# Performance work log

Measured on AMD Instinct MI355X. Metric: run time of the kernel, lower is better.

## Reference

```python
import jax, jax.numpy as jnp
import numpy as np
import math

N = 524288          # number of 3D query points
L = 4               # grid_level = num_sin_layers - 2
F = 8               # feat_dim per hash level
T = 1 << 19         # log2_hashmap_size = 19 (hardcoded in module)
H = 64              # SIREN hidden width (dims entries)
OUT_DIM = 128       # sin_dims[-1] * size_factor
BOUND = 1.0
BASE_RES = 16.0
PER_LEVEL_SCALE = 2.0
BASE_SIGMA = 5.0
EXP_SIGMA = 2.0
SIN_W0 = 30.0
SIN_W1 = 30.0

_PRIMES = jnp.array([1, 2654435761, 805459861], dtype=jnp.uint32)  # tcnn hash primes
_CORNERS = np.array([[(i >> 2) & 1, (i >> 1) & 1, i & 1] for i in range(8)])
_CORNERS_U = jnp.asarray(_CORNERS, dtype=jnp.uint32)
_CORNERS_F = jnp.asarray(_CORNERS, dtype=jnp.float32)


def hash_grid(pos01, table):
    """Multi-resolution hash-grid encoding. pos01: [N,3] in [0,1], table: [L,T,F] -> [L,N,F]."""
    res = jnp.floor(BASE_RES * PER_LEVEL_SCALE ** jnp.arange(L, dtype=jnp.float32))  # [L]

    def level(tab, r):
        p = pos01 * r                       # [N,3]
        p0 = jnp.floor(p)
        f = p - p0                          # trilinear fractions
        c = p0.astype(jnp.uint32)[:, None, :] + _CORNERS_U[None]   # [N,8,3] corner coords
        hp = c * _PRIMES
        h = (hp[..., 0] ^ hp[..., 1] ^ hp[..., 2]) & jnp.uint32(T - 1)  # [N,8] hash indices
        feats = tab[h]                      # [N,8,F]
        w = jnp.prod(jnp.where(_CORNERS_F[None] > 0, f[:, None, :], 1.0 - f[:, None, :]), axis=-1)  # [N,8]
        return jnp.einsum('nc,ncf->nf', w, feats)

    return jax.vmap(level)(table, res)


def setup_inputs() -> dict:
    key = jax.random.key(0)
    ks = jax.random.split(key, 10)
    in_pos = jax.random.uniform(ks[0], (N, 3), minval=-BOUND, maxval=BOUND)
    table = jax.random.uniform(ks[1], (L, T, F), minval=-1e-4, maxval=1e-4)
    # ffn[i] = randn(F, H) * base_sigma * exp_sigma**i
    scales = BASE_SIGMA * EXP_SIGMA ** jnp.arange(L, dtype=jnp.float32)
    ffn = jax.random.normal(ks[2], (L, F, H)) * scales[:, None, None]
    # SIREN init: first layer U(-1/fan_in, 1/fan_in); others U(-sqrt(6/fan_in)/w0, ...)
    W0 = jax.random.uniform(ks[3], (3, H), minval=-1.0 / 3.0, maxval=1.0 / 3.0)
    b0 = jax.random.uniform(ks[4], (H,), minval=-1.0 / math.sqrt(3.0), maxval=1.0 / math.sqrt(3.0))
    bw = math.sqrt(6.0 / H) / SIN_W0
    Ws = jax.random.uniform(ks[5], (L, H, H), minval=-bw, maxval=bw)
    bs = jax.random.uniform(ks[6], (L, H), minval=-1.0 / math.sqrt(H), maxval=1.0 / math.sqrt(H))
    bo = math.sqrt(6.0 / H) / SIN_W1
    Wout = jax.random.uniform(ks[7], (L, H, OUT_DIM), minval=-bo, maxval=bo)
    bout = jax.random.uniform(ks[8], (L, OUT_DIM), minval=-1.0 / math.sqrt(H), maxval=1.0 / math.sqrt(H))
    return {"in_pos": in_pos, "table": table, "ffn": ffn, "W0": W0, "b0": b0,
            "Ws": Ws, "bs": bs, "Wout": Wout, "bout": bout}


def reference(in_pos, table, ffn, W0, b0, Ws, bs, Wout, bout):
    x = in_pos / BOUND                              # SIREN input in [-1,1]
    pos01 = (in_pos + BOUND) / (2.0 * BOUND)        # grid input in [0,1]
    grid_x = hash_grid(pos01, table)                # [L,N,F]
    # Fourier feature branch: sin(2*pi * grid_x @ ffn)
    emb = jnp.sin(2.0 * math.pi * jnp.einsum('lnf,lfh->lnh', grid_x, ffn))  # [L,N,H]
    # first SIREN layer (layer 0)
    x = jnp.sin(SIN_W0 * (x @ W0 + b0))             # [N,H]
    x_out = jnp.zeros((x.shape[0], OUT_DIM), x.dtype)
    for l in range(L):                              # layers 1..num_sin_layers-2
        x = jnp.sin(SIN_W0 * (x @ Ws[l] + bs[l]))
        x = emb[l] + x                              # residual add of grid Fourier features
        x_out = x_out + jnp.sin(SIN_W1 * (x @ Wout[l] + bout[l]))  # accumulate output head
    return x_out
```

## Files before the change

kernel.cpp:

```cpp
#include <hip/hip_runtime.h>
#include <cstdint>
#include <cstddef>

#define NLVL 4
#define TSIZE (1u << 19)
#define NH 64
#define NOUT 128
#define MBLK 128
#define PANEL 12800

typedef _Float16 f16x8 __attribute__((ext_vector_type(8)));
typedef _Float16 f16x2 __attribute__((ext_vector_type(2)));
typedef float f32x4 __attribute__((ext_vector_type(4)));
typedef unsigned short u16x8 __attribute__((ext_vector_type(8)));
typedef unsigned int u32x4 __attribute__((ext_vector_type(4)));

__device__ __forceinline__ float fsin_rad(float x) {
    return __builtin_amdgcn_sinf(__builtin_amdgcn_fractf(x * 0.15915494309189535f));
}
__device__ __forceinline__ float fsin_rev(float r) {
    return __builtin_amdgcn_sinf(__builtin_amdgcn_fractf(r));
}
__device__ __forceinline__ unsigned short h2u(_Float16 h) {
    return __builtin_bit_cast(unsigned short, h);
}
__device__ __forceinline__ unsigned int pk16(float a, float b) {
    return __builtin_bit_cast(unsigned int, __builtin_amdgcn_cvt_pkrtz(a, b));
}
__device__ __forceinline__ void gl_lds16(const _Float16* g, _Float16* l) {
    __builtin_amdgcn_global_load_lds(
        (const __attribute__((address_space(1))) void*)g,
        (__attribute__((address_space(3))) void*)l, 16, 0, 0);
}

__global__ void prep_weights(const float* __restrict__ Ws,
                             const float* __restrict__ Wout,
                             const float* __restrict__ ffn,
                             _Float16* __restrict__ ws)
{
    int i = blockIdx.x * 256 + threadIdx.x;
    if (i < 16384) {
        int l = i >> 12, r = i & 4095, k = r >> 6, c = r & 63;
        ws[l * PANEL + ((c * 64 + k) ^ ((c & 7) << 3))] = (_Float16)Ws[i];
    } else if (i < 18432) {
        int j = i - 16384;
        int l = j >> 9, r = j & 511, k = r >> 6, c = r & 63;
        ws[l * PANEL + 4096 + c * 8 + k] = (_Float16)ffn[j];
    } else if (i < 51200) {
        int j = i - 18432;
        int l = j >> 13, rem = j & 8191, k = rem >> 7, c = rem & 127;
        int ct = c >> 4, r15 = c & 15, kb = k >> 5, hi4 = (k >> 3) & 3, jj = k & 7;
        ws[l * PANEL + 4608 + (ct * 2 + kb) * 512 + hi4 * 128 + r15 * 8 + jj] =
            (_Float16)Wout[j];
    }
}

__global__ __launch_bounds__(256) void prep_table(const float* __restrict__ table,
                                                  _Float16* __restrict__ tab16)
{
    int i = blockIdx.x * 256 + threadIdx.x;
    float v = __builtin_nontemporal_load(table + i);
    tab16[i] = (_Float16)(v * 4096.f);
}

template <bool F16TAB>
__global__ __launch_bounds__(512, 2)
void ffb_main(const float* __restrict__ in_pos,
              const float* __restrict__ table,
              const _Float16* __restrict__ tab16,
              const float* __restrict__ W0,
              const float* __restrict__ b0,
              const float* __restrict__ bs,
              const float* __restrict__ bout,
              const _Float16* __restrict__ wsg,
              float* __restrict__ out)
{
    __shared__ __align__(16) _Float16 wbuf[2][PANEL];
    __shared__ __align__(16) unsigned short gS[NLVL][MBLK][8];

    const int tid = threadIdx.x;
    const int pbase = blockIdx.x * MBLK;
    const int lane = tid & 63;
    const int wv = tid >> 6;
    const int r15 = lane & 15;
    const int hi4 = lane >> 4;

    {
        const int p = tid & (MBLK - 1);
        const int lv = tid >> 7;
        const float px = in_pos[3 * (pbase + p) + 0];
        const float py = in_pos[3 * (pbase + p) + 1];
        const float pz = in_pos[3 * (pbase + p) + 2];
        const float qx = (px + 1.f) * 0.5f, qy = (py + 1.f) * 0.5f, qz = (pz + 1.f) * 0.5f;
        const uint32_t P1 = 2654435761u, P2 = 805459861u;

        const float res = (float)(16 << lv);
        float gx = qx * res, gy = qy * res, gz = qz * res;
        float fx0 = floorf(gx), fy0 = floorf(gy), fz0 = floorf(gz);
        float fx = gx - fx0, fy = gy - fy0, fz = gz - fz0;
        uint32_t ux = (uint32_t)fx0, uy = (uint32_t)fy0, uz = (uint32_t)fz0;
        uint32_t hx0 = ux, hx1 = ux + 1u;
        uint32_t hy0 = uy * P1, hy1 = hy0 + P1;
        uint32_t hz0 = uz * P2, hz1 = hz0 + P2;

        uint32_t hh[8];
        float    wgt[8];
        #pragma unroll
        for (int c = 0; c < 8; ++c) {
            hh[c] = (((c & 4) ? hx1 : hx0) ^ ((c & 2) ? hy1 : hy0)
                     ^ ((c & 1) ? hz1 : hz0)) & (TSIZE - 1u);
            wgt[c] = ((c & 4) ? fx : 1.f - fx) * ((c & 2) ? fy : 1.f - fy)
                   * ((c & 1) ? fz : 1.f - fz);
        }

        if (F16TAB) {
            const _Float16* tl = tab16 + (size_t)lv * TSIZE * 8;
            u16x8 vv[8];
            #pragma unroll
            for (int c = 0; c < 8; ++c)
                vv[c] = *(const u16x8*)(tl + (size_t)hh[c] * 8);
            f16x2 acc2[4];
            #pragma unroll
            for (int q = 0; q < 4; ++q) acc2[q] = (f16x2){(_Float16)0.f, (_Float16)0.f};
            #pragma unroll
            for (int c = 0; c < 8; ++c) {
                _Float16 wh = (_Float16)wgt[c];
                f16x2 ww = {wh, wh};
                const f16x2* vp = (const f16x2*)&vv[c];
                #pragma unroll
                for (int q = 0; q < 4; ++q) acc2[q] = acc2[q] + ww * vp[q];
            }
            *(u16x8*)&gS[lv][p][0] = *(u16x8*)&acc2[0];
        } else {
            const float* tl = table + (size_t)lv * TSIZE * 8;
            float g[8];
            #pragma unroll
            for (int q = 0; q < 8; ++q) g[q] = 0.f;
            #pragma unroll
            for (int c = 0; c < 8; ++c) {
                const float4* fp = (const float4*)(tl + (size_t)hh[c] * 8);
                float4 va = fp[0], vb = fp[1];
                float w = wgt[c];
                g[0] = fmaf(w, va.x, g[0]); g[1] = fmaf(w, va.y, g[1]);
                g[2] = fmaf(w, va.z, g[2]); g[3] = fmaf(w, va.w, g[3]);
                g[4] = fmaf(w, vb.x, g[4]); g[5] = fmaf(w, vb.y, g[5]);
                g[6] = fmaf(w, vb.z, g[6]); g[7] = fmaf(w, vb.w, g[7]);
            }
            u16x8 gv;
            #pragma unroll
            for (int q = 0; q < 8; ++q)
                gv[q] = h2u((_Float16)(g[q] * 4096.f));
            *(u16x8*)&gS[lv][p][0] = gv;
        }
    }

    auto stage = [&](int l) {
        const _Float16* src = wsg + l * PANEL;
        _Float16* dst = &wbuf[l & 1][0];
        #pragma unroll
        for (int i = 0; i < 3; ++i)
            gl_lds16(src + (i * 512 + tid) * 8, dst + (i * 512 + (tid & ~63)) * 8);
        if (tid < 64)
            gl_lds16(src + (1536 + tid) * 8, dst + 1536 * 8);
    };
    stage(0);

    f16x8 Xb[2];
    {
        const int pp = pbase + wv * 16 + r15;
        const float lpx = in_pos[3 * pp + 0];
        const float lpy = in_pos[3 * pp + 1];
        const float lpz = in_pos[3 * pp + 2];
        #pragma unroll
        for (int kb = 0; kb < 2; ++kb) {
            f16x8 v;
            #pragma unroll
            for (int j = 0; j < 8; ++j) {
                const int f = kb * 32 + hi4 * 8 + j;
                float a = b0[f] + lpx * W0[f] + lpy * W0[64 + f] + lpz * W0[128 + f];
                v[j] = (_Float16)fsin_rad(30.f * a);
            }
            Xb[kb] = v;
        }
    }
    __syncthreads();

    const int idxA = ((lane & 16) << 3) + r15 * 4;
    const int idxB = idxA + 64;
    const bool hiHalf = (lane & 32) != 0;

    f16x2 accP[8][2];
    #pragma unroll
    for (int ct = 0; ct < 8; ++ct)
        #pragma unroll
        for (int s = 0; s < 2; ++s) accP[ct][s] = (f16x2){(_Float16)0.f, (_Float16)0.f};

    #pragma unroll 1
    for (int lvl = 0; lvl < NLVL; ++lvl) {
        if (lvl < NLVL - 1) stage(lvl + 1);
        const _Float16* wp = &wbuf[lvl & 1][0];

        f16x8 gB;
        {
            f16x8 z;
            #pragma unroll
            for (int q = 0; q < 8; ++q) z[q] = (_Float16)0.f;
            if (lane < 16)
                z = *(const f16x8*)&gS[lvl][wv * 16 + lane][0];
            gB = z;
        }

        unsigned int P[4][2];
        #pragma unroll
        for (int ct = 0; ct < 4; ++ct) {
            const int i0 = ((ct * 16 + r15) * 64 + hi4 * 8) ^ ((r15 & 7) << 3);
            f16x8 A0 = *(const f16x8*)&wp[i0];
            f16x8 A1 = *(const f16x8*)&wp[i0 ^ 32];
            f16x8 Af;
            #pragma unroll
            for (int q = 0; q < 8; ++q) Af[q] = (_Float16)0.f;
            if (lane < 16)
                Af = *(const f16x8*)&wp[4096 + (ct * 16 + lane) * 8];
            float4 bs4 = *(const float4*)&bs[lvl * 64 + ct * 16 + hi4 * 4];

            f32x4 c1 = {0.f, 0.f, 0.f, 0.f};
            c1 = __builtin_amdgcn_mfma_f32_16x16x32_f16(A0, Xb[0], c1, 0, 0, 0);
            c1 = __builtin_amdgcn_mfma_f32_16x16x32_f16(A1, Xb[1], c1, 0, 0, 0);
            f32x4 c2 = {0.f, 0.f, 0.f, 0.f};
            c2 = __builtin_amdgcn_mfma_f32_16x16x32_f16(Af, gB, c2, 0, 0, 0);

            float xn0 = fsin_rad(30.f * (c1[0] + bs4.x)) + fsin_rev(c2[0] * 0.000244140625f);
            float xn1 = fsin_rad(30.f * (c1[1] + bs4.y)) + fsin_rev(c2[1] * 0.000244140625f);
            float xn2 = fsin_rad(30.f * (c1[2] + bs4.z)) + fsin_rev(c2[2] * 0.000244140625f);
            float xn3 = fsin_rad(30.f * (c1[3] + bs4.w)) + fsin_rev(c2[3] * 0.000244140625f);
            P[ct][0] = pk16(xn0, xn1);
            P[ct][1] = pk16(xn2, xn3);
        }

        #pragma unroll
        for (int kb = 0; kb < 2; ++kb) {
            unsigned int w[4];
            #pragma unroll
            for (int m = 0; m < 4; ++m) {
                int idx = (m < 2) ? idxA : idxB;
                int lo = __builtin_amdgcn_ds_bpermute(idx, (int)P[2 * kb + 0][m & 1]);
                int hi = __builtin_amdgcn_ds_bpermute(idx, (int)P[2 * kb + 1][m & 1]);
                w[m] = (unsigned int)(hiHalf ? hi : lo);
            }
            Xb[kb] = __builtin_bit_cast(f16x8, (u32x4){w[0], w[1], w[2], w[3]});
        }

        #pragma unroll
        for (int ct = 0; ct < 8; ++ct) {
            const _Float16* bp = &wp[4608 + (ct * 2) * 512 + hi4 * 128 + r15 * 8];
            f16x8 B0 = *(const f16x8*)bp;
            f16x8 B1 = *(const f16x8*)(bp + 512);
            float bov = bout[lvl * 128 + ct * 16 + r15];
            f32x4 c = {0.f, 0.f, 0.f, 0.f};
            c = __builtin_amdgcn_mfma_f32_16x16x32_f16(Xb[0], B0, c, 0, 0, 0);
            c = __builtin_amdgcn_mfma_f32_16x16x32_f16(Xb[1], B1, c, 0, 0, 0);
            float s0 = fsin_rad(30.f * (c[0] + bov));
            float s1 = fsin_rad(30.f * (c[1] + bov));
            float s2 = fsin_rad(30.f * (c[2] + bov));
            float s3 = fsin_rad(30.f * (c[3] + bov));
            accP[ct][0] = accP[ct][0] + __builtin_bit_cast(f16x2, pk16(s0, s1));
            accP[ct][1] = accP[ct][1] + __builtin_bit_cast(f16x2, pk16(s2, s3));
        }

        if (lvl < NLVL - 1) __syncthreads();
    }

    #pragma unroll
    for (int s = 0; s < 2; ++s)
        #pragma unroll
        for (int r2 = 0; r2 < 2; ++r2) {
            int row = pbase + wv * 16 + hi4 * 4 + s * 2 + r2;
            #pragma unroll
            for (int ct = 0; ct < 8; ++ct) {
                float v = (float)accP[ct][s][r2];
                __builtin_nontemporal_store(v, &out[(size_t)row * 128 + ct * 16 + r15]);
            }
        }
}

extern "C" void kernel_launch(void* const* d_in, const int* in_sizes, int n_in,
                              void* d_out, int out_size, void* d_ws, size_t ws_size,
                              hipStream_t stream) {
    const float* in_pos = (const float*)d_in[0];
    const float* table  = (const float*)d_in[1];
    const float* ffn    = (const float*)d_in[2];
    const float* W0     = (const float*)d_in[3];
    const float* b0     = (const float*)d_in[4];
    const float* Ws     = (const float*)d_in[5];
    const float* bs     = (const float*)d_in[6];
    const float* Wout   = (const float*)d_in[7];
    const float* bout   = (const float*)d_in[8];
    float* out = (float*)d_out;
    _Float16* ws = (_Float16*)d_ws;

    const size_t need = 65536u * 2u + (size_t)NLVL * TSIZE * 8u * 2u;
    const bool f16tab = (ws_size >= need);
    _Float16* tab16 = ws + 65536;

    prep_weights<<<dim3(200), dim3(256), 0, stream>>>(Ws, Wout, ffn, ws);

    const int n = in_sizes[0] / 3;
    if (f16tab) {
        prep_table<<<dim3((NLVL * TSIZE * 8) / 256), dim3(256), 0, stream>>>(table, tab16);
        ffb_main<true><<<dim3(n / MBLK), dim3(512), 0, stream>>>(
            in_pos, table, tab16, W0, b0, bs, bout, ws, out);
    } else {
        ffb_main<false><<<dim3(n / MBLK), dim3(512), 0, stream>>>(
            in_pos, table, tab16, W0, b0, bs, bout, ws, out);
    }
}
```

Baseline: 255.2 us.

## Software-pipeline hidden-layer and output-head phases with split LDS buffers

Splits the per-level weight panel into separate double-buffered LDS regions for the hidden/Fourier weights and the output-head weights. The level loop is restructured so the hidden-layer MFMAs of level l+1 are interleaved with the output-head MFMAs of level l, with weights prefetched up to two levels ahead. The aim is to break the serial dependency within each level and overlap LDS, MFMA and transcendental work. Launch bounds are also raised to request 4 blocks per CU, which caps registers per thread and risks spills, while the LDS footprint likely still limits residency to about 2 blocks.

```diff
diff --git a/kernel.cpp b/kernel.cpp
--- a/kernel.cpp
+++ b/kernel.cpp
@@ -64,7 +64,7 @@
 }
 
 template <bool F16TAB>
-__global__ __launch_bounds__(512, 2)
+__global__ __launch_bounds__(512, 4)
 void ffb_main(const float* __restrict__ in_pos,
               const float* __restrict__ table,
               const _Float16* __restrict__ tab16,
@@ -75,7 +75,8 @@
               const _Float16* __restrict__ wsg,
               float* __restrict__ out)
 {
-    __shared__ __align__(16) _Float16 wbuf[2][PANEL];
+    __shared__ __align__(16) _Float16 wsf[2][4608];
+    __shared__ __align__(16) _Float16 wob[2][8192];
     __shared__ __align__(16) unsigned short gS[NLVL][MBLK][8];
 
     const int tid = threadIdx.x;
@@ -154,16 +155,22 @@
         }
     }
 
-    auto stage = [&](int l) {
+    auto stageWsf = [&](int l) {
         const _Float16* src = wsg + l * PANEL;
-        _Float16* dst = &wbuf[l & 1][0];
-        #pragma unroll
-        for (int i = 0; i < 3; ++i)
-            gl_lds16(src + (i * 512 + tid) * 8, dst + (i * 512 + (tid & ~63)) * 8);
-        if (tid < 64)
-            gl_lds16(src + (1536 + tid) * 8, dst + 1536 * 8);
-    };
-    stage(0);
+        _Float16* dst = &wsf[l & 1][0];
+        gl_lds16(src + tid * 8, dst + (tid & ~63) * 8);
+        if (tid < 64) gl_lds16(src + 4096 + tid * 8, dst + 4096);
+    };
+    auto stageWob = [&](int l) {
+        const _Float16* src = wsg + l * PANEL + 4608;
+        _Float16* dst = &wob[l & 1][0];
+        gl_lds16(src + tid * 8, dst + (tid & ~63) * 8);
+        gl_lds16(src + 4096 + tid * 8, dst + 4096 + (tid & ~63) * 8);
+    };
+
+    stageWsf(0);
+    stageWsf(1);
+    stageWob(0);
 
     f16x8 Xb[2];
     {
@@ -195,11 +202,7 @@
         #pragma unroll
         for (int s = 0; s < 2; ++s) accP[ct][s] = (f16x2){(_Float16)0.f, (_Float16)0.f};
 
-    #pragma unroll 1
-    for (int lvl = 0; lvl < NLVL; ++lvl) {
-        if (lvl < NLVL - 1) stage(lvl + 1);
-        const _Float16* wp = &wbuf[lvl & 1][0];
-
+    auto phaseB = [&](int lvl, const _Float16* wp, unsigned int P[4][2]) {
         f16x8 gB;
         {
             f16x8 z;
@@ -209,8 +212,6 @@
                 z = *(const f16x8*)&gS[lvl][wv * 16 + lane][0];
             gB = z;
         }
-
-        unsigned int P[4][2];
         #pragma unroll
         for (int ct = 0; ct < 4; ++ct) {
             const int i0 = ((ct * 16 + r15) * 64 + hi4 * 8) ^ ((r15 & 7) << 3);
@@ -236,7 +237,8 @@
             P[ct][0] = pk16(xn0, xn1);
             P[ct][1] = pk16(xn2, xn3);
         }
-
+    };
+    auto exchange = [&](unsigned int P[4][2]) {
         #pragma unroll
         for (int kb = 0; kb < 2; ++kb) {
             unsigned int w[4];
@@ -249,16 +251,17 @@
             }
             Xb[kb] = __builtin_bit_cast(f16x8, (u32x4){w[0], w[1], w[2], w[3]});
         }
-
+    };
+    auto phaseC = [&](int lvl, const _Float16* wp, const f16x8 Xc[2]) {
         #pragma unroll
         for (int ct = 0; ct < 8; ++ct) {
-            const _Float16* bp = &wp[4608 + (ct * 2) * 512 + hi4 * 128 + r15 * 8];
+            const _Float16* bp = &wp[(ct * 2) * 512 + hi4 * 128 + r15 * 8];
             f16x8 B0 = *(const f16x8*)bp;
             f16x8 B1 = *(const f16x8*)(bp + 512);
             float bov = bout[lvl * 128 + ct * 16 + r15];
             f32x4 c = {0.f, 0.f, 0.f, 0.f};
-            c = __builtin_amdgcn_mfma_f32_16x16x32_f16(Xb[0], B0, c, 0, 0, 0);
-            c = __builtin_amdgcn_mfma_f32_16x16x32_f16(Xb[1], B1, c, 0, 0, 0);
+            c = __builtin_amdgcn_mfma_f32_16x16x32_f16(Xc[0], B0, c, 0, 0, 0);
+            c = __builtin_amdgcn_mfma_f32_16x16x32_f16(Xc[1], B1, c, 0, 0, 0);
             float s0 = fsin_rad(30.f * (c[0] + bov));
             float s1 = fsin_rad(30.f * (c[1] + bov));
             float s2 = fsin_rad(30.f * (c[2] + bov));
@@ -266,9 +269,29 @@
             accP[ct][0] = accP[ct][0] + __builtin_bit_cast(f16x2, pk16(s0, s1));
             accP[ct][1] = accP[ct][1] + __builtin_bit_cast(f16x2, pk16(s2, s3));
         }
-
-        if (lvl < NLVL - 1) __syncthreads();
-    }
+    };
+
+    {
+        unsigned int P[4][2];
+        phaseB(0, &wsf[0][0], P);
+        exchange(P);
+    }
+    __syncthreads();
+
+    #pragma unroll 1
+    for (int l = 0; l < NLVL - 1; ++l) {
+        if (l < 2) stageWsf(l + 2);
+        stageWob(l + 1);
+
+        f16x8 Xc[2] = {Xb[0], Xb[1]};
+        unsigned int P[4][2];
+        phaseB(l + 1, &wsf[(l + 1) & 1][0], P);
+        phaseC(l, &wob[l & 1][0], Xc);
+        exchange(P);
+        __syncthreads();
+    }
+
+    phaseC(3, &wob[1][0], Xb);
 
     #pragma unroll
     for (int s = 0; s < 2; ++s)
```

Measured after the change: 264.5 us. 3.7% more time.
